# Kernel optimization log

Measured on AMD Instinct MI355X. Metric: run time of the kernel, lower is better.

## Reference

```python
import jax, jax.numpy as jnp
import numpy as np

B, C, H, W = 4, 256, 256, 512
MAXLOAD = 100


def setup_inputs() -> dict:
    key = jax.random.key(0)
    kf, kx, kw, ky, kh = jax.random.split(key, 5)
    features = jax.random.normal(kf, (B, C, H, W), dtype=jnp.float32)
    # ROIs in original-image coords (image is 2048x1024); x0 > 0 so all ROIs are 'valid'
    x0 = jax.random.uniform(kx, (B, MAXLOAD), minval=1.0, maxval=1200.0)
    bw = jax.random.uniform(kw, (B, MAXLOAD), minval=16.0, maxval=800.0)
    x1 = jnp.minimum(x0 + bw, 2047.0)
    y0 = jax.random.uniform(ky, (B, MAXLOAD), minval=1.0, maxval=600.0)
    bh = jax.random.uniform(kh, (B, MAXLOAD), minval=16.0, maxval=400.0)
    y1 = jnp.minimum(y0 + bh, 1023.0)
    rois = jnp.stack([x0, y0, x1, y1], axis=-1).astype(jnp.float32)  # [B, maxLoad, 4]
    return {"features": features, "rois": rois, "shrink_scale": 4,
            "image_height": 1024, "feature_size": 14}


def reference(features, rois, shrink_scale, image_height, feature_size):
    b, c, h, w = features.shape
    max_load = rois.shape[1]
    fs = feature_size
    dscale = float(shrink_scale)

    rois_flat = rois.reshape(-1, 4)                       # [B*maxLoad, 4]
    val_bind = jnp.repeat(jnp.arange(b), max_load)        # indicator; all ROIs valid by construction
    n = rois_flat.shape[0]

    # per-ROI sampling grids in (shrunken) stacked-image coordinates
    ar = jnp.arange(fs, dtype=jnp.float32)
    xx, yy = jnp.meshgrid(ar, ar, indexing='xy')          # [fs, fs]
    biasx = rois_flat[:, 0]
    scalex = rois_flat[:, 2] - rois_flat[:, 0]
    biasy = rois_flat[:, 1] + val_bind.astype(jnp.float32) * float(image_height)
    scaley = rois_flat[:, 3] - rois_flat[:, 1]
    gridxx = (xx[None] / (fs - 1) * scalex[:, None, None] + biasx[:, None, None]) / dscale  # [N, fs, fs]
    gridyy = (yy[None] / (fs - 1) * scaley[:, None, None] + biasy[:, None, None]) / dscale

    # stack batch along height: [C, B*H, W]
    feats = features.transpose(1, 0, 2, 3).reshape(c, b * h, w)
    hb = b * h

    # normalize as in module, then unnormalize per grid_sample(align_corners=False)
    gx = (gridxx / (w - 1) - 0.5) * 2.0
    gy = (gridyy / (hb - 1) - 0.5) * 2.0
    px = ((gx + 1.0) * w - 1.0) * 0.5
    py = ((gy + 1.0) * hb - 1.0) * 0.5
    # padding_mode='border': clip coordinates
    px = jnp.clip(px, 0.0, w - 1.0)
    py = jnp.clip(py, 0.0, hb - 1.0)

    x0f = jnp.floor(px); y0f = jnp.floor(py)
    wx = px - x0f; wy = py - y0f                           # [N, fs, fs]
    x0i = x0f.astype(jnp.int32); y0i = y0f.astype(jnp.int32)
    x1i = jnp.minimum(x0i + 1, w - 1); y1i = jnp.minimum(y0i + 1, hb - 1)

    f00 = feats[:, y0i, x0i]                               # [C, N, fs, fs]
    f01 = feats[:, y0i, x1i]
    f10 = feats[:, y1i, x0i]
    f11 = feats[:, y1i, x1i]
    wxb = wx[None]; wyb = wy[None]
    out = (f00 * (1 - wxb) * (1 - wyb) + f01 * wxb * (1 - wyb)
           + f10 * (1 - wxb) * wyb + f11 * wxb * wyb)      # [C, N, fs, fs]
    out = out.transpose(1, 0, 2, 3)                        # [N, C, fs, fs]
    return out, val_bind
```

## Files before the change

kernel.cpp:

```cpp
#include <hip/hip_runtime.h>

constexpr int B = 4, C = 256, H = 256, W = 512;
constexpr int MAXLOAD = 100, FS = 14;
constexpr int NROI = B * MAXLOAD;
constexpr int HB = B * H;
constexpr int MAIN = NROI * C * FS * FS;
constexpr int TOTAL = MAIN + NROI;

__global__ __launch_bounds__(256) void pooler_kernel(
    const float* __restrict__ feats,
    const float* __restrict__ rois,
    float* __restrict__ out)
{
    int idx = blockIdx.x * 256 + threadIdx.x;
    if (idx >= TOTAL) return;

    if (idx >= MAIN) {
        int n = idx - MAIN;
        out[idx] = (float)(n / MAXLOAD);
        return;
    }

    int r  = idx % (FS * FS);
    int q  = idx / (FS * FS);
    int fx = r % FS;
    int fy = r / FS;
    int c  = q & (C - 1);
    int n  = q >> 8;
    int vb = n / MAXLOAD;

    float4 roi = reinterpret_cast<const float4*>(rois)[n];
    float scalex = roi.z - roi.x;
    float scaley = roi.w - roi.y;
    float biasx  = roi.x;
    float biasy  = roi.y + (float)vb * 1024.0f;

    float gridx = ((float)fx * (1.0f / 13.0f) * scalex + biasx) * 0.25f;
    float gridy = ((float)fy * (1.0f / 13.0f) * scaley + biasy) * 0.25f;

    float px = gridx * (512.0f / 511.0f) - 0.5f;
    float py = gridy * (1024.0f / 1023.0f) - 0.5f;
    px = fminf(fmaxf(px, 0.0f), (float)(W - 1));
    py = fminf(fmaxf(py, 0.0f), (float)(HB - 1));

    float x0f = floorf(px), y0f = floorf(py);
    float wx = px - x0f, wy = py - y0f;
    int x0 = (int)x0f, y0 = (int)y0f;
    int x1 = min(x0 + 1, W - 1);
    int y1 = min(y0 + 1, HB - 1);

    int cb  = c * (H * W);
    int ro0 = ((y0 >> 8) * (C * H) + (y0 & (H - 1))) * W + cb;
    int ro1 = ((y1 >> 8) * (C * H) + (y1 & (H - 1))) * W + cb;

    float f00 = feats[ro0 + x0];
    float f01 = feats[ro0 + x1];
    float f10 = feats[ro1 + x0];
    float f11 = feats[ro1 + x1];

    float v0 = f00 + wx * (f01 - f00);
    float v1 = f10 + wx * (f11 - f10);
    out[idx] = v0 + wy * (v1 - v0);
}

extern "C" void kernel_launch(void* const* d_in, const int* in_sizes, int n_in,
                              void* d_out, int out_size, void* d_ws, size_t ws_size,
                              hipStream_t stream) {
    const float* feats = (const float*)d_in[0];
    const float* rois  = (const float*)d_in[1];
    float* out = (float*)d_out;

    int blocks = (TOTAL + 255) / 256;
    pooler_kernel<<<blocks, 256, 0, stream>>>(feats, rois, out);
}
```

Baseline: 747.7 us.

## Stage ROI feature rows in shared memory per ROI-channel block

Each block now handles one (ROI, channel) pair. It first loads the 28 needed feature rows over the ROI's x-span into LDS with coalesced float4 reads, then does the bilinear interpolation from shared memory. This replaces four scattered global gathers per output with contiguous row loads. The trade-offs are that it may fetch columns between samples that are never used, and only 196 of 256 threads do the compute phase.

New measurement: 868.9 us. +16.2%, slower.

```diff
diff --git a/kernel.cpp b/kernel.cpp
--- a/kernel.cpp
+++ b/kernel.cpp
@@ -5,62 +5,87 @@
 constexpr int NROI = B * MAXLOAD;
 constexpr int HB = B * H;
 constexpr int MAIN = NROI * C * FS * FS;
-constexpr int TOTAL = MAIN + NROI;
+constexpr int NROWS = 2 * FS;
+constexpr int STRIDE = 212;
 
-__global__ __launch_bounds__(256) void pooler_kernel(
+__global__ __launch_bounds__(256) void pooler_stage_kernel(
     const float* __restrict__ feats,
     const float* __restrict__ rois,
     float* __restrict__ out)
 {
-    int idx = blockIdx.x * 256 + threadIdx.x;
-    if (idx >= TOTAL) return;
+    __shared__ float buf[NROWS * STRIDE];
 
-    if (idx >= MAIN) {
-        int n = idx - MAIN;
-        out[idx] = (float)(n / MAXLOAD);
-        return;
+    const int blk = blockIdx.x;
+    const int c   = blk & (C - 1);
+    const int n   = blk >> 8;
+    const int vb  = n / MAXLOAD;
+    const int tid = threadIdx.x;
+
+    const float4 roi = reinterpret_cast<const float4*>(rois)[n];
+    const float scalex = roi.z - roi.x;
+    const float scaley = roi.w - roi.y;
+    const float biasx  = roi.x;
+    const float biasy  = roi.y + (float)vb * 1024.0f;
+
+    auto PX = [&](int fx) {
+        float g = ((float)fx * (1.0f / 13.0f) * scalex + biasx) * 0.25f;
+        float p = g * (512.0f / 511.0f) - 0.5f;
+        return fminf(fmaxf(p, 0.0f), 511.0f);
+    };
+    auto PY = [&](int fy) {
+        float g = ((float)fy * (1.0f / 13.0f) * scaley + biasy) * 0.25f;
+        float p = g * (1024.0f / 1023.0f) - 0.5f;
+        return fminf(fmaxf(p, 0.0f), 1023.0f);
+    };
+
+    const int x_lo  = (int)floorf(PX(0));
+    const int x_hi  = min((int)floorf(PX(13)) + 1, W - 1);
+    const int xbase = x_lo & ~3;
+    const int span4 = ((x_hi - xbase) >> 2) + 1;
+    const int total = NROWS * span4;
+    const int cb    = c * (H * W);
+
+    for (int t = tid; t < total; t += 256) {
+        int i  = t / span4;
+        int j  = t - i * span4;
+        int fy = (i < FS) ? i : i - FS;
+        int y0 = (int)floorf(PY(fy));
+        int y  = (i < FS) ? y0 : min(y0 + 1, HB - 1);
+        int rowbase = ((y >> 8) * (C * H) + (y & (H - 1))) * W + cb;
+        int col = xbase + (j << 2);
+        float4 v;
+        if (col + 3 < W) {
+            v = *reinterpret_cast<const float4*>(feats + rowbase + col);
+        } else {
+            v.x = feats[rowbase + min(col,     W - 1)];
+            v.y = feats[rowbase + min(col + 1, W - 1)];
+            v.z = feats[rowbase + min(col + 2, W - 1)];
+            v.w = feats[rowbase + min(col + 3, W - 1)];
+        }
+        *reinterpret_cast<float4*>(&buf[i * STRIDE + (j << 2)]) = v;
     }
 
-    int r  = idx % (FS * FS);
-    int q  = idx / (FS * FS);
-    int fx = r % FS;
-    int fy = r / FS;
-    int c  = q & (C - 1);
-    int n  = q >> 8;
-    int vb = n / MAXLOAD;
+    __syncthreads();
 
-    float4 roi = reinterpret_cast<const float4*>(rois)[n];
-    float scalex = roi.z - roi.x;
-    float scaley = roi.w - roi.y;
-    float biasx  = roi.x;
-    float biasy  = roi.y + (float)vb * 1024.0f;
-
-    float gridx = ((float)fx * (1.0f / 13.0f) * scalex + biasx) * 0.25f;
-    float gridy = ((float)fy * (1.0f / 13.0f) * scaley + biasy) * 0.25f;
-
-    float px = gridx * (512.0f / 511.0f) - 0.5f;
-    float py = gridy * (1024.0f / 1023.0f) - 0.5f;
-    px = fminf(fmaxf(px, 0.0f), (float)(W - 1));
-    py = fminf(fmaxf(py, 0.0f), (float)(HB - 1));
-
-    float x0f = floorf(px), y0f = floorf(py);
-    float wx = px - x0f, wy = py - y0f;
-    int x0 = (int)x0f, y0 = (int)y0f;
-    int x1 = min(x0 + 1, W - 1);
-    int y1 = min(y0 + 1, HB - 1);
-
-    int cb  = c * (H * W);
-    int ro0 = ((y0 >> 8) * (C * H) + (y0 & (H - 1))) * W + cb;
-    int ro1 = ((y1 >> 8) * (C * H) + (y1 & (H - 1))) * W + cb;
-
-    float f00 = feats[ro0 + x0];
-    float f01 = feats[ro0 + x1];
-    float f10 = feats[ro1 + x0];
-    float f11 = feats[ro1 + x1];
-
-    float v0 = f00 + wx * (f01 - f00);
-    float v1 = f10 + wx * (f11 - f10);
-    out[idx] = v0 + wy * (v1 - v0);
+    if (tid < FS * FS) {
+        int fx = tid % FS;
+        int fy = tid / FS;
+        float px = PX(fx);
+        float py = PY(fy);
+        float x0f = floorf(px), y0f = floorf(py);
+        float wx = px - x0f,   wy = py - y0f;
+        int x0 = (int)x0f - xbase;
+        int x1 = min((int)x0f + 1, W - 1) - xbase;
+        const float* r0 = &buf[fy * STRIDE];
+        const float* r1 = &buf[(fy + FS) * STRIDE];
+        float f00 = r0[x0], f01 = r0[x1];
+        float f10 = r1[x0], f11 = r1[x1];
+        float v0 = f00 + wx * (f01 - f00);
+        float v1 = f10 + wx * (f11 - f10);
+        out[(size_t)blk * (FS * FS) + tid] = v0 + wy * (v1 - v0);
+    } else if (c == 0 && tid == 255) {
+        out[MAIN + n] = (float)vb;
+    }
 }
 
 extern "C" void kernel_launch(void* const* d_in, const int* in_sizes, int n_in,
@@ -70,6 +95,5 @@
     const float* rois  = (const float*)d_in[1];
     float* out = (float*)d_out;
 
-    int blocks = (TOTAL + 255) / 256;
-    pooler_kernel<<<blocks, 256, 0, stream>>>(feats, rois, out);
+    pooler_stage_kernel<<<NROI * C, 256, 0, stream>>>(feats, rois, out);
 }
```
